# Kernel optimization log

Measured on AMD Instinct MI355X. Metric: run time of the kernel, lower is better.

Reference implementation:

```python
import jax
import jax.numpy as jnp
from jax import lax
import numpy as np

VOCAB = 50000
EMB = 32
HID = 32
LAYERS = 4
BATCH = 8192
SEQ = 111


def setup_inputs() -> dict:
    key = jax.random.key(0)
    ks = jax.random.split(key, 12)
    s = 0.1
    x = jax.random.randint(ks[0], (BATCH, SEQ), 0, VOCAB, dtype=jnp.int64 if jax.config.read('jax_enable_x64') else jnp.int32)
    emb = jax.random.normal(ks[1], (VOCAB, EMB), jnp.float32) * s
    # stacked per-layer LSTM weights; layer-0 input dim == EMB == HID so stacking is valid
    Wih = jax.random.normal(ks[2], (LAYERS, 4 * HID, EMB), jnp.float32) * s
    Whh = jax.random.normal(ks[3], (LAYERS, 4 * HID, HID), jnp.float32) * s
    bih = jax.random.normal(ks[4], (LAYERS, 4 * HID), jnp.float32) * s
    bhh = jax.random.normal(ks[5], (LAYERS, 4 * HID), jnp.float32) * s
    Wa = jax.random.normal(ks[6], (HID, 1), jnp.float32) * s
    ba = jax.random.normal(ks[7], (1,), jnp.float32) * s
    W1 = jax.random.normal(ks[8], (HID, 32), jnp.float32) * s
    b1 = jax.random.normal(ks[9], (32,), jnp.float32) * s
    W2 = jax.random.normal(ks[10], (32, 3), jnp.float32) * s
    b2 = jax.random.normal(ks[11], (3,), jnp.float32) * s
    return {"x": x, "emb": emb, "Wih": Wih, "Whh": Whh, "bih": bih, "bhh": bhh,
            "Wa": Wa, "ba": ba, "W1": W1, "b1": b1, "W2": W2, "b2": b2}


def _lstm_layer(x, Wih, Whh, bih, bhh):
    # x: [B, T, D] -> [B, T, H]; PyTorch gate order: i, f, g, o
    B = x.shape[0]
    H = Whh.shape[1]
    # precompute the input contribution for all timesteps (one big GEMM)
    xg = jnp.einsum('btd,gd->btg', x, Wih) + bih + bhh  # [B, T, 4H]

    def step(carry, xg_t):
        h, c = carry
        z = xg_t + h @ Whh.T  # [B, 4H]
        i, f, g, o = jnp.split(z, 4, axis=-1)
        c = jax.nn.sigmoid(f) * c + jax.nn.sigmoid(i) * jnp.tanh(g)
        h = jax.nn.sigmoid(o) * jnp.tanh(c)
        return (h, c), h

    init = (jnp.zeros((B, H), x.dtype), jnp.zeros((B, H), x.dtype))
    _, hs = lax.scan(step, init, jnp.swapaxes(xg, 0, 1))  # hs: [T, B, H]
    return jnp.swapaxes(hs, 0, 1)


def reference(x, emb, Wih, Whh, bih, bhh, Wa, ba, W1, b1, W2, b2):
    h = emb[x]  # [B, T, E]
    for l in range(Wih.shape[0]):  # fixed 4 layers
        h = _lstm_layer(h, Wih[l], Whh[l], bih[l], bhh[l])
    scores = h @ Wa + ba                       # [B, T, 1]
    attn = jax.nn.softmax(scores, axis=1)      # softmax over time
    context = jnp.sum(h * attn, axis=1)        # [B, H]
    hid = jnp.tanh(context @ W1 + b1)          # dropout is identity at eval
    return hid @ W2 + b2                       # [B, 3]
```

## Files before the change

kernel.cpp:

```cpp
#include <hip/hip_runtime.h>

#define TSEQ 111
#define L2E 1.44269504088896340736f
#define TWO_L2E 2.88539008177792680472f

using f32x4  = __attribute__((ext_vector_type(4))) float;
using f32x2  = __attribute__((ext_vector_type(2))) float;
using short8 = __attribute__((ext_vector_type(8))) short;

union FragU { unsigned u[4]; uint4 v; short8 s; };

__device__ __forceinline__ float fexp2(float x) { return __builtin_amdgcn_exp2f(x); }
__device__ __forceinline__ float frcp(float x)  { return __builtin_amdgcn_rcpf(x); }
__device__ __forceinline__ float tanh2(float zs) { return 1.f - 2.f * frcp(1.f + fexp2(zs + zs)); }
__device__ __forceinline__ f32x2 exp2v(f32x2 x) { f32x2 r; r[0] = fexp2(x[0]); r[1] = fexp2(x[1]); return r; }
__device__ __forceinline__ f32x2 rcpv(f32x2 x)  { f32x2 r; r[0] = frcp(x[0]); r[1] = frcp(x[1]); return r; }

__device__ __forceinline__ unsigned rnd_bf16(float w) {
  unsigned u = __float_as_uint(w);
  return (u + 0x7fffu + ((u >> 16) & 1u)) >> 16;
}
__device__ __forceinline__ unsigned cvtpk(float a, float b) {
  unsigned r;
  asm("v_cvt_pk_bf16_f32 %0, %1, %2" : "=v"(r) : "v"(a), "v"(b));
  return r;
}

__global__ __launch_bounds__(512, 4) void lstm_fused(
    const int* __restrict__ x, const float* __restrict__ emb,
    const float* __restrict__ Wih, const float* __restrict__ Whh,
    const float* __restrict__ bih, const float* __restrict__ bhh,
    const float* __restrict__ Wa, const float* __restrict__ W1,
    const float* __restrict__ b1, const float* __restrict__ W2,
    const float* __restrict__ b2, float* __restrict__ out)
{
  __shared__ __align__(16) unsigned short hb[2 * 4 * 512];

  const int tid  = threadIdx.x;
  const int wvu  = __builtin_amdgcn_readfirstlane(tid) >> 6;
  const int l    = wvu >> 1;
  const int hf   = wvu & 1;
  const int lane = tid & 63;
  const int c    = lane & 15;
  const int q    = lane >> 4;
  const int gcc  = (c & 3) ^ (c >> 2);
  const int rowbase = blockIdx.x * 16;
  const int xrow = (rowbase + c) * TSEQ;

  const int rdOff = c * 32 + ((q ^ gcc) << 3);
  const int wrOff = c * 32 + ((((2 * hf + (q >> 1)) ^ gcc) << 3) | ((q & 1) << 2));

  FragU wihf[4], whhf[4];
#pragma unroll
  for (int g = 0; g < 4; ++g) {
    const float sj = (g == 2) ? TWO_L2E : -L2E;
    const int wr = 32 * g + 16 * hf + c;
    const float* srcI = Wih + l * 4096 + wr * 32 + 8 * q;
    const float* srcH = Whh + l * 4096 + wr * 32 + 8 * q;
#pragma unroll
    for (int p = 0; p < 4; ++p) {
      wihf[g].u[p] = rnd_bf16(srcI[2 * p] * sj) | (rnd_bf16(srcI[2 * p + 1] * sj) << 16);
      whhf[g].u[p] = rnd_bf16(srcH[2 * p] * sj) | (rnd_bf16(srcH[2 * p + 1] * sj) << 16);
    }
  }
  f32x4 bvv[4];
#pragma unroll
  for (int g = 0; g < 4; ++g) {
    const float sj = (g == 2) ? TWO_L2E : -L2E;
    const int bi = l * 128 + 32 * g + 16 * hf + 4 * q;
#pragma unroll
    for (int e = 0; e < 4; ++e)
      bvv[g][e] = (bih[bi + e] + bhh[bi + e]) * sj;
  }

  FragU wahA, walA;
#pragma unroll
  for (int p = 0; p < 4; ++p) { wahA.u[p] = 0u; walA.u[p] = 0u; }
  if (l == 3) {
#pragma unroll
    for (int p = 0; p < 4; ++p) {
      const int k0 = 8 * q + 2 * p;
      float w0 = Wa[k0] * L2E, w1 = Wa[k0 + 1] * L2E;
      unsigned h0 = rnd_bf16(w0), h1b = rnd_bf16(w1);
      wahA.u[p] = h0 | (h1b << 16);
      float l0v = w0 - __uint_as_float(h0 << 16);
      float l1v = w1 - __uint_as_float(h1b << 16);
      walA.u[p] = rnd_bf16(l0v) | (rnd_bf16(l1v) << 16);
    }
  }

  f32x2 cs2[2];
  cs2[0] = (f32x2){0.f, 0.f}; cs2[1] = (f32x2){0.f, 0.f};
  float mr = -1e30f, sr = 0.f, cx[4];
#pragma unroll
  for (int e = 0; e < 4; ++e) cx[e] = 0.f;

  for (int i = tid; i < 2 * 4 * 512 / 2; i += 512) ((unsigned*)hb)[i] = 0u;

  float4 emA = make_float4(0.f, 0.f, 0.f, 0.f), emB = emA;
  int idxn = 0;
  if (l == 0) {
    int i0 = x[xrow];
    emA = *(const float4*)(emb + i0 * 32 + 8 * q);
    emB = *(const float4*)(emb + i0 * 32 + 8 * q + 4);
    idxn = x[xrow + 1];
  }
  __syncthreads();

  if (blockIdx.x & 1) {
    __builtin_amdgcn_s_sleep(15);
    __builtin_amdgcn_s_sleep(15);
  }

#pragma unroll 2
  for (int s = 0; s < TSEQ + 4; ++s) {
    const int t = s - l;
    const bool active = ((unsigned)t < (unsigned)TSEQ);
    const int rp = (s + 1) & 1;
    const int wp = s & 1;
    const bool doAtt = (l == 3) && (s >= 4);

    FragU fi, fh;
    __builtin_amdgcn_s_setprio(1);
    if (active) {
      if (l == 0) {
        fi.u[0] = cvtpk(emA.x, emA.y); fi.u[1] = cvtpk(emA.z, emA.w);
        fi.u[2] = cvtpk(emB.x, emB.y); fi.u[3] = cvtpk(emB.z, emB.w);
        if (t + 1 < TSEQ) {
          emA = *(const float4*)(emb + idxn * 32 + 8 * q);
          emB = *(const float4*)(emb + idxn * 32 + 8 * q + 4);
        }
        if (t + 2 < TSEQ) idxn = x[xrow + t + 2];
      } else {
        fi.v = *(const uint4*)(hb + (rp * 4 + (l - 1)) * 512 + rdOff);
      }
    }
    if (active || doAtt)
      fh.v = *(const uint4*)(hb + (rp * 4 + l) * 512 + rdOff);

    f32x4 acc[4];
    if (active) {
#pragma unroll
      for (int g = 0; g < 4; ++g) {
        acc[g] = __builtin_amdgcn_mfma_f32_16x16x32_bf16(wihf[g].s, fi.s, bvv[g], 0, 0, 0);
        acc[g] = __builtin_amdgcn_mfma_f32_16x16x32_bf16(whhf[g].s, fh.s, acc[g], 0, 0, 0);
      }
    }
    f32x4 sacc;
    if (doAtt) {
      f32x4 z = {0.f, 0.f, 0.f, 0.f};
      sacc = __builtin_amdgcn_mfma_f32_16x16x32_bf16(wahA.s, fh.s, z, 0, 0, 0);
      sacc = __builtin_amdgcn_mfma_f32_16x16x32_bf16(walA.s, fh.s, sacc, 0, 0, 0);
    }
    __builtin_amdgcn_s_setprio(0);

    if (active) {
      float hv[4];
      const f32x2 one = {1.f, 1.f};
      const f32x2 tl2 = {TWO_L2E, TWO_L2E};
#pragma unroll
      for (int pr2 = 0; pr2 < 2; ++pr2) {
        const int e0 = 2 * pr2;
        f32x2 va; va[0] = acc[0][e0]; va[1] = acc[0][e0 + 1];
        f32x2 vm; vm[0] = acc[1][e0]; vm[1] = acc[1][e0 + 1];
        f32x2 vb; vb[0] = acc[2][e0]; vb[1] = acc[2][e0 + 1];
        f32x2 vp; vp[0] = acc[3][e0]; vp[1] = acc[3][e0 + 1];
        f32x2 ea = exp2v(va), em_ = exp2v(vm), eb = exp2v(vb), ep = exp2v(vp);
        f32x2 P  = (one + ea) * (one + eb);
        f32x2 M1 = one + em_;
        f32x2 num = cs2[pr2] * P + (eb - one) * M1;
        f32x2 cn = num * rcpv(M1 * P);
        cs2[pr2] = cn;
        f32x2 qa = cn * tl2;
        qa[0] = fminf(qa[0], 80.f); qa[1] = fminf(qa[1], 80.f);
        f32x2 qv = exp2v(qa);
        f32x2 hvv = (qv - one) * rcpv((one + ep) * (one + qv));
        hv[e0] = hvv[0]; hv[e0 + 1] = hvv[1];
      }

      *(uint2*)(hb + (wp * 4 + l) * 512 + wrOff) =
          make_uint2(cvtpk(hv[0], hv[1]), cvtpk(hv[2], hv[3]));
    }

    if (doAtt) {
      float pf = sacc[0];
      float mn = fmaxf(mr, pf);
      float sc = fexp2(mr - mn);
      float pr = fexp2(pf - mn);
      sr = sr * sc + pr;
#pragma unroll
      for (int p = 0; p < 2; ++p) {
        unsigned w = fh.u[2 * hf + p];
        cx[2 * p]     = cx[2 * p]     * sc + pr * __uint_as_float(w << 16);
        cx[2 * p + 1] = cx[2 * p + 1] * sc + pr * __uint_as_float(w & 0xffff0000u);
      }
      mr = mn;
    }

    asm volatile("s_waitcnt lgkmcnt(0)\n\ts_barrier" ::: "memory");
  }

  __syncthreads();

  float* cb = (float*)hb;
  if (l == 3) {
    float inv = frcp(sr);
#pragma unroll
    for (int e = 0; e < 4; ++e)
      cb[c * 33 + 8 * q + 4 * hf + e] = cx[e] * inv;
  }
  __syncthreads();
  if (wvu != 6) return;

  float a0[4], a1[4];
  {
    float bb0 = b1[c], bb1 = b1[c + 16];
#pragma unroll
    for (int e = 0; e < 4; ++e) { a0[e] = bb0; a1[e] = bb1; }
    for (int j = 0; j < 32; ++j) {
      float w0 = W1[j * 32 + c];
      float w1 = W1[j * 32 + c + 16];
#pragma unroll
      for (int e = 0; e < 4; ++e) {
        float cr = cb[(4 * q + e) * 33 + j];
        a0[e] = fmaf(cr, w0, a0[e]);
        a1[e] = fmaf(cr, w1, a1[e]);
      }
    }
  }
  float o0[4], o1[4], o2[4];
  {
    float w20 = W2[c * 3 + 0], w21 = W2[c * 3 + 1], w22 = W2[c * 3 + 2];
    float w30 = W2[(c + 16) * 3 + 0], w31 = W2[(c + 16) * 3 + 1], w32 = W2[(c + 16) * 3 + 2];
#pragma unroll
    for (int e = 0; e < 4; ++e) {
      float h0 = tanh2(a0[e] * L2E);
      float hB = tanh2(a1[e] * L2E);
      o0[e] = h0 * w20 + hB * w30;
      o1[e] = h0 * w21 + hB * w31;
      o2[e] = h0 * w22 + hB * w32;
    }
  }
#pragma unroll
  for (int mk = 1; mk <= 8; mk <<= 1) {
#pragma unroll
    for (int e = 0; e < 4; ++e) {
      o0[e] += __shfl_xor(o0[e], mk, 64);
      o1[e] += __shfl_xor(o1[e], mk, 64);
      o2[e] += __shfl_xor(o2[e], mk, 64);
    }
  }
  if (c < 3) {
    float bb = b2[c];
#pragma unroll
    for (int e = 0; e < 4; ++e) {
      float v = (c == 0) ? o0[e] : ((c == 1) ? o1[e] : o2[e]);
      out[(rowbase + 4 * q + e) * 3 + c] = v + bb;
    }
  }
}

extern "C" void kernel_launch(void* const* d_in, const int* in_sizes, int n_in,
                              void* d_out, int out_size, void* d_ws, size_t ws_size,
                              hipStream_t stream) {
  const int*   x   = (const int*)d_in[0];
  const float* emb = (const float*)d_in[1];
  const float* Wih = (const float*)d_in[2];
  const float* Whh = (const float*)d_in[3];
  const float* bih = (const float*)d_in[4];
  const float* bhh = (const float*)d_in[5];
  const float* Wa  = (const float*)d_in[6];
  const float* W1  = (const float*)d_in[8];
  const float* b1  = (const float*)d_in[9];
  const float* W2  = (const float*)d_in[10];
  const float* b2  = (const float*)d_in[11];
  float* out = (float*)d_out;

  lstm_fused<<<512, 512, 0, stream>>>(x, emb, Wih, Whh, bih, bhh, Wa, W1, b1, W2, b2, out);
}
```

Before: 164.5 us.

## Process LSTM layers in 8-timestep chunks with one wave per layer

Each layer is now handled by a single wave that keeps the recurrent state in registers. Hidden states pass between layers through shared memory in chunks of 8 timesteps, so the block barriers drop from one per timestep to one per chunk. The block shrinks from 512 to 256 threads, and the per-layer wave pair and swizzled LDS layout go away, along with the s_sleep staggering and setprio. In exchange each wave does twice the MFMA and transcendental work per step, serially, with higher register pressure. The skew between layers is now a whole chunk, and the last chunk is padded.

```diff
diff --git a/kernel.cpp b/kernel.cpp
--- a/kernel.cpp
+++ b/kernel.cpp
@@ -1,6 +1,9 @@
 #include <hip/hip_runtime.h>
 
 #define TSEQ 111
+#define CT 8
+#define NCH 14
+#define NSS (NCH + 3)
 #define L2E 1.44269504088896340736f
 #define TWO_L2E 2.88539008177792680472f
 
@@ -20,13 +23,16 @@
   unsigned u = __float_as_uint(w);
   return (u + 0x7fffu + ((u >> 16) & 1u)) >> 16;
 }
+__device__ __forceinline__ unsigned pk2(float a, float b) {
+  return rnd_bf16(a) | (rnd_bf16(b) << 16);
+}
 __device__ __forceinline__ unsigned cvtpk(float a, float b) {
   unsigned r;
   asm("v_cvt_pk_bf16_f32 %0, %1, %2" : "=v"(r) : "v"(a), "v"(b));
   return r;
 }
 
-__global__ __launch_bounds__(512, 4) void lstm_fused(
+__global__ __launch_bounds__(256, 2) void lstm_fused(
     const int* __restrict__ x, const float* __restrict__ emb,
     const float* __restrict__ Wih, const float* __restrict__ Whh,
     const float* __restrict__ bih, const float* __restrict__ bhh,
@@ -34,40 +40,33 @@
     const float* __restrict__ b1, const float* __restrict__ W2,
     const float* __restrict__ b2, float* __restrict__ out)
 {
-  __shared__ __align__(16) unsigned short hb[2 * 4 * 512];
+  __shared__ __align__(16) unsigned short buf[2 * 3 * CT * 512];
 
   const int tid  = threadIdx.x;
-  const int wvu  = __builtin_amdgcn_readfirstlane(tid) >> 6;
-  const int l    = wvu >> 1;
-  const int hf   = wvu & 1;
+  const int l    = __builtin_amdgcn_readfirstlane(tid) >> 6;
   const int lane = tid & 63;
   const int c    = lane & 15;
   const int q    = lane >> 4;
-  const int gcc  = (c & 3) ^ (c >> 2);
   const int rowbase = blockIdx.x * 16;
   const int xrow = (rowbase + c) * TSEQ;
 
-  const int rdOff = c * 32 + ((q ^ gcc) << 3);
-  const int wrOff = c * 32 + ((((2 * hf + (q >> 1)) ^ gcc) << 3) | ((q & 1) << 2));
-
-  FragU wihf[4], whhf[4];
-#pragma unroll
-  for (int g = 0; g < 4; ++g) {
-    const float sj = (g == 2) ? TWO_L2E : -L2E;
-    const int wr = 32 * g + 16 * hf + c;
-    const float* srcI = Wih + l * 4096 + wr * 32 + 8 * q;
-    const float* srcH = Whh + l * 4096 + wr * 32 + 8 * q;
-#pragma unroll
-    for (int p = 0; p < 4; ++p) {
-      wihf[g].u[p] = rnd_bf16(srcI[2 * p] * sj) | (rnd_bf16(srcI[2 * p + 1] * sj) << 16);
-      whhf[g].u[p] = rnd_bf16(srcH[2 * p] * sj) | (rnd_bf16(srcH[2 * p + 1] * sj) << 16);
-    }
-  }
-  f32x4 bvv[4];
-#pragma unroll
-  for (int g = 0; g < 4; ++g) {
-    const float sj = (g == 2) ? TWO_L2E : -L2E;
-    const int bi = l * 128 + 32 * g + 16 * hf + 4 * q;
+  FragU wih[8], whh[8];
+  f32x4 bvv[8];
+#pragma unroll
+  for (int g = 0; g < 8; ++g) {
+    const float sj = ((g >> 1) == 2) ? TWO_L2E : -L2E;
+    const int wr = 16 * g + c;
+    const float* WI = Wih + l * 4096 + wr * 32;
+    const float* WH = Whh + l * 4096 + wr * 32;
+    float4 ia = *(const float4*)(WI + 4 * q);
+    float4 ib = *(const float4*)(WI + 16 + 4 * q);
+    float4 ha = *(const float4*)(WH + 4 * q);
+    float4 hb = *(const float4*)(WH + 16 + 4 * q);
+    wih[g].u[0] = pk2(ia.x * sj, ia.y * sj); wih[g].u[1] = pk2(ia.z * sj, ia.w * sj);
+    wih[g].u[2] = pk2(ib.x * sj, ib.y * sj); wih[g].u[3] = pk2(ib.z * sj, ib.w * sj);
+    whh[g].u[0] = pk2(ha.x * sj, ha.y * sj); whh[g].u[1] = pk2(ha.z * sj, ha.w * sj);
+    whh[g].u[2] = pk2(hb.x * sj, hb.y * sj); whh[g].u[3] = pk2(hb.z * sj, hb.w * sj);
+    const int bi = l * 128 + 16 * g + 4 * q;
 #pragma unroll
     for (int e = 0; e < 4; ++e)
       bvv[g][e] = (bih[bi + e] + bhh[bi + e]) * sj;
@@ -77,140 +76,178 @@
 #pragma unroll
   for (int p = 0; p < 4; ++p) { wahA.u[p] = 0u; walA.u[p] = 0u; }
   if (l == 3) {
+    float wv[8];
+    float4 wa0 = *(const float4*)(Wa + 4 * q);
+    float4 wa1 = *(const float4*)(Wa + 16 + 4 * q);
+    wv[0] = wa0.x; wv[1] = wa0.y; wv[2] = wa0.z; wv[3] = wa0.w;
+    wv[4] = wa1.x; wv[5] = wa1.y; wv[6] = wa1.z; wv[7] = wa1.w;
 #pragma unroll
     for (int p = 0; p < 4; ++p) {
-      const int k0 = 8 * q + 2 * p;
-      float w0 = Wa[k0] * L2E, w1 = Wa[k0 + 1] * L2E;
-      unsigned h0 = rnd_bf16(w0), h1b = rnd_bf16(w1);
-      wahA.u[p] = h0 | (h1b << 16);
+      float w0 = wv[2 * p] * L2E, w1 = wv[2 * p + 1] * L2E;
+      unsigned h0 = rnd_bf16(w0), h1 = rnd_bf16(w1);
+      wahA.u[p] = h0 | (h1 << 16);
       float l0v = w0 - __uint_as_float(h0 << 16);
-      float l1v = w1 - __uint_as_float(h1b << 16);
+      float l1v = w1 - __uint_as_float(h1 << 16);
       walA.u[p] = rnd_bf16(l0v) | (rnd_bf16(l1v) << 16);
     }
   }
 
-  f32x2 cs2[2];
-  cs2[0] = (f32x2){0.f, 0.f}; cs2[1] = (f32x2){0.f, 0.f};
-  float mr = -1e30f, sr = 0.f, cx[4];
-#pragma unroll
-  for (int e = 0; e < 4; ++e) cx[e] = 0.f;
-
-  for (int i = tid; i < 2 * 4 * 512 / 2; i += 512) ((unsigned*)hb)[i] = 0u;
-
-  float4 emA = make_float4(0.f, 0.f, 0.f, 0.f), emB = emA;
-  int idxn = 0;
+  f32x2 csE[2], csO[2];
+  csE[0] = (f32x2){0.f, 0.f}; csE[1] = (f32x2){0.f, 0.f};
+  csO[0] = (f32x2){0.f, 0.f}; csO[1] = (f32x2){0.f, 0.f};
+  FragU fh;
+  fh.u[0] = 0u; fh.u[1] = 0u; fh.u[2] = 0u; fh.u[3] = 0u;
+  float mr = -1e30f, sr = 0.f;
+  float cxE[4], cxO[4];
+#pragma unroll
+  for (int e = 0; e < 4; ++e) { cxE[e] = 0.f; cxO[e] = 0.f; }
+
+  int idxc[CT];
   if (l == 0) {
-    int i0 = x[xrow];
-    emA = *(const float4*)(emb + i0 * 32 + 8 * q);
-    emB = *(const float4*)(emb + i0 * 32 + 8 * q + 4);
-    idxn = x[xrow + 1];
+#pragma unroll
+    for (int j = 0; j < CT; ++j) idxc[j] = x[xrow + j];
   }
   __syncthreads();
 
-  if (blockIdx.x & 1) {
-    __builtin_amdgcn_s_sleep(15);
-    __builtin_amdgcn_s_sleep(15);
-  }
-
-#pragma unroll 2
-  for (int s = 0; s < TSEQ + 4; ++s) {
-    const int t = s - l;
-    const bool active = ((unsigned)t < (unsigned)TSEQ);
+  for (int s = 0; s < NSS; ++s) {
+    const int ch = s - l;
+    const bool active = ((unsigned)ch < (unsigned)NCH);
     const int rp = (s + 1) & 1;
     const int wp = s & 1;
-    const bool doAtt = (l == 3) && (s >= 4);
-
-    FragU fi, fh;
-    __builtin_amdgcn_s_setprio(1);
+
+    FragU fiU[CT];
+    float4 emE[4], emO[4];
+    int idxn[CT];
+
+    if (l == 0) {
+      if (active) {
+#pragma unroll
+        for (int j = 0; j < 4; ++j) {
+          emE[j] = *(const float4*)(emb + idxc[j] * 32 + 4 * q);
+          emO[j] = *(const float4*)(emb + idxc[j] * 32 + 16 + 4 * q);
+        }
+#pragma unroll
+        for (int j = 0; j < CT; ++j) {
+          int tt = (ch + 1) * CT + j;
+          tt = tt > TSEQ - 1 ? TSEQ - 1 : tt;
+          idxn[j] = x[xrow + tt];
+        }
+      }
+    } else if (active) {
+      const unsigned short* bp =
+          buf + ((rp * 3 + (l - 1)) * CT) * 512 + c * 32 + q * 8;
+#pragma unroll
+      for (int j = 0; j < CT; ++j)
+        fiU[j].v = *(const uint4*)(bp + j * 512);
+    }
+
     if (active) {
+#pragma unroll
+      for (int tau = 0; tau < CT; ++tau) {
+        FragU fi;
+        if (l == 0) {
+          float4 eE = emE[tau & 3], eO = emO[tau & 3];
+          fi.u[0] = cvtpk(eE.x, eE.y); fi.u[1] = cvtpk(eE.z, eE.w);
+          fi.u[2] = cvtpk(eO.x, eO.y); fi.u[3] = cvtpk(eO.z, eO.w);
+          if (tau + 4 < CT) {
+            emE[tau & 3] = *(const float4*)(emb + idxc[tau + 4] * 32 + 4 * q);
+            emO[tau & 3] = *(const float4*)(emb + idxc[tau + 4] * 32 + 16 + 4 * q);
+          }
+        } else {
+          fi = fiU[tau];
+        }
+
+        f32x4 acc[8];
+#pragma unroll
+        for (int g = 0; g < 8; ++g)
+          acc[g] = __builtin_amdgcn_mfma_f32_16x16x32_bf16(wih[g].s, fi.s, bvv[g], 0, 0, 0);
+#pragma unroll
+        for (int g = 0; g < 8; ++g)
+          acc[g] = __builtin_amdgcn_mfma_f32_16x16x32_bf16(whh[g].s, fh.s, acc[g], 0, 0, 0);
+
+        float hvE[4], hvO[4];
+        const f32x2 one = {1.f, 1.f};
+        const f32x2 tl2 = {TWO_L2E, TWO_L2E};
+#pragma unroll
+        for (int p2 = 0; p2 < 2; ++p2) {
+          const int e0 = 2 * p2;
+          {
+            f32x2 vi; vi[0] = acc[0][e0]; vi[1] = acc[0][e0 + 1];
+            f32x2 vf; vf[0] = acc[2][e0]; vf[1] = acc[2][e0 + 1];
+            f32x2 vg; vg[0] = acc[4][e0]; vg[1] = acc[4][e0 + 1];
+            f32x2 vo; vo[0] = acc[6][e0]; vo[1] = acc[6][e0 + 1];
+            f32x2 ea = exp2v(vi), em_ = exp2v(vf), eb = exp2v(vg), ep = exp2v(vo);
+            f32x2 P  = (one + ea) * (one + eb);
+            f32x2 M1 = one + em_;
+            f32x2 cn = (csE[p2] * P + (eb - one) * M1) * rcpv(M1 * P);
+            csE[p2] = cn;
+            f32x2 qa = cn * tl2;
+            qa[0] = fminf(qa[0], 80.f); qa[1] = fminf(qa[1], 80.f);
+            f32x2 qv = exp2v(qa);
+            f32x2 hvv = (qv - one) * rcpv((one + ep) * (one + qv));
+            hvE[e0] = hvv[0]; hvE[e0 + 1] = hvv[1];
+          }
+          {
+            f32x2 vi; vi[0] = acc[1][e0]; vi[1] = acc[1][e0 + 1];
+            f32x2 vf; vf[0] = acc[3][e0]; vf[1] = acc[3][e0 + 1];
+            f32x2 vg; vg[0] = acc[5][e0]; vg[1] = acc[5][e0 + 1];
+            f32x2 vo; vo[0] = acc[7][e0]; vo[1] = acc[7][e0 + 1];
+            f32x2 ea = exp2v(vi), em_ = exp2v(vf), eb = exp2v(vg), ep = exp2v(vo);
+            f32x2 P  = (one + ea) * (one + eb);
+            f32x2 M1 = one + em_;
+            f32x2 cn = (csO[p2] * P + (eb - one) * M1) * rcpv(M1 * P);
+            csO[p2] = cn;
+            f32x2 qa = cn * tl2;
+            qa[0] = fminf(qa[0], 80.f); qa[1] = fminf(qa[1], 80.f);
+            f32x2 qv = exp2v(qa);
+            f32x2 hvv = (qv - one) * rcpv((one + ep) * (one + qv));
+            hvO[e0] = hvv[0]; hvO[e0 + 1] = hvv[1];
+          }
+        }
+
+        fh.u[0] = cvtpk(hvE[0], hvE[1]); fh.u[1] = cvtpk(hvE[2], hvE[3]);
+        fh.u[2] = cvtpk(hvO[0], hvO[1]); fh.u[3] = cvtpk(hvO[2], hvO[3]);
+
+        if (l < 3)
+          *(uint4*)(buf + ((wp * 3 + l) * CT + tau) * 512 + c * 32 + q * 8) = fh.v;
+
+        if (l == 3 && ch * CT + tau < TSEQ) {
+          f32x4 z = {0.f, 0.f, 0.f, 0.f};
+          f32x4 sacc = __builtin_amdgcn_mfma_f32_16x16x32_bf16(wahA.s, fh.s, z, 0, 0, 0);
+          sacc = __builtin_amdgcn_mfma_f32_16x16x32_bf16(walA.s, fh.s, sacc, 0, 0, 0);
+          float pf = sacc[0];
+          float mn = fmaxf(mr, pf);
+          float scl = fexp2(mr - mn);
+          float pr = fexp2(pf - mn);
+          sr = sr * scl + pr;
+#pragma unroll
+          for (int e = 0; e < 4; ++e) {
+            cxE[e] = cxE[e] * scl + pr * hvE[e];
+            cxO[e] = cxO[e] * scl + pr * hvO[e];
+          }
+          mr = mn;
+        }
+      }
       if (l == 0) {
-        fi.u[0] = cvtpk(emA.x, emA.y); fi.u[1] = cvtpk(emA.z, emA.w);
-        fi.u[2] = cvtpk(emB.x, emB.y); fi.u[3] = cvtpk(emB.z, emB.w);
-        if (t + 1 < TSEQ) {
-          emA = *(const float4*)(emb + idxn * 32 + 8 * q);
-          emB = *(const float4*)(emb + idxn * 32 + 8 * q + 4);
-        }
-        if (t + 2 < TSEQ) idxn = x[xrow + t + 2];
-      } else {
-        fi.v = *(const uint4*)(hb + (rp * 4 + (l - 1)) * 512 + rdOff);
+#pragma unroll
+        for (int j = 0; j < CT; ++j) idxc[j] = idxn[j];
       }
     }
-    if (active || doAtt)
-      fh.v = *(const uint4*)(hb + (rp * 4 + l) * 512 + rdOff);
-
-    f32x4 acc[4];
-    if (active) {
-#pragma unroll
-      for (int g = 0; g < 4; ++g) {
-        acc[g] = __builtin_amdgcn_mfma_f32_16x16x32_bf16(wihf[g].s, fi.s, bvv[g], 0, 0, 0);
-        acc[g] = __builtin_amdgcn_mfma_f32_16x16x32_bf16(whhf[g].s, fh.s, acc[g], 0, 0, 0);
-      }
-    }
-    f32x4 sacc;
-    if (doAtt) {
-      f32x4 z = {0.f, 0.f, 0.f, 0.f};
-      sacc = __builtin_amdgcn_mfma_f32_16x16x32_bf16(wahA.s, fh.s, z, 0, 0, 0);
-      sacc = __builtin_amdgcn_mfma_f32_16x16x32_bf16(walA.s, fh.s, sacc, 0, 0, 0);
-    }
-    __builtin_amdgcn_s_setprio(0);
-
-    if (active) {
-      float hv[4];
-      const f32x2 one = {1.f, 1.f};
-      const f32x2 tl2 = {TWO_L2E, TWO_L2E};
-#pragma unroll
-      for (int pr2 = 0; pr2 < 2; ++pr2) {
-        const int e0 = 2 * pr2;
-        f32x2 va; va[0] = acc[0][e0]; va[1] = acc[0][e0 + 1];
-        f32x2 vm; vm[0] = acc[1][e0]; vm[1] = acc[1][e0 + 1];
-        f32x2 vb; vb[0] = acc[2][e0]; vb[1] = acc[2][e0 + 1];
-        f32x2 vp; vp[0] = acc[3][e0]; vp[1] = acc[3][e0 + 1];
-        f32x2 ea = exp2v(va), em_ = exp2v(vm), eb = exp2v(vb), ep = exp2v(vp);
-        f32x2 P  = (one + ea) * (one + eb);
-        f32x2 M1 = one + em_;
-        f32x2 num = cs2[pr2] * P + (eb - one) * M1;
-        f32x2 cn = num * rcpv(M1 * P);
-        cs2[pr2] = cn;
-        f32x2 qa = cn * tl2;
-        qa[0] = fminf(qa[0], 80.f); qa[1] = fminf(qa[1], 80.f);
-        f32x2 qv = exp2v(qa);
-        f32x2 hvv = (qv - one) * rcpv((one + ep) * (one + qv));
-        hv[e0] = hvv[0]; hv[e0 + 1] = hvv[1];
-      }
-
-      *(uint2*)(hb + (wp * 4 + l) * 512 + wrOff) =
-          make_uint2(cvtpk(hv[0], hv[1]), cvtpk(hv[2], hv[3]));
-    }
-
-    if (doAtt) {
-      float pf = sacc[0];
-      float mn = fmaxf(mr, pf);
-      float sc = fexp2(mr - mn);
-      float pr = fexp2(pf - mn);
-      sr = sr * sc + pr;
-#pragma unroll
-      for (int p = 0; p < 2; ++p) {
-        unsigned w = fh.u[2 * hf + p];
-        cx[2 * p]     = cx[2 * p]     * sc + pr * __uint_as_float(w << 16);
-        cx[2 * p + 1] = cx[2 * p + 1] * sc + pr * __uint_as_float(w & 0xffff0000u);
-      }
-      mr = mn;
-    }
 
     asm volatile("s_waitcnt lgkmcnt(0)\n\ts_barrier" ::: "memory");
   }
 
-  __syncthreads();
-
-  float* cb = (float*)hb;
+  float* cb = (float*)buf;
   if (l == 3) {
     float inv = frcp(sr);
 #pragma unroll
-    for (int e = 0; e < 4; ++e)
-      cb[c * 33 + 8 * q + 4 * hf + e] = cx[e] * inv;
+    for (int e = 0; e < 4; ++e) {
+      cb[c * 33 + 4 * q + e]      = cxE[e] * inv;
+      cb[c * 33 + 16 + 4 * q + e] = cxO[e] * inv;
+    }
   }
   __syncthreads();
-  if (wvu != 6) return;
+  if (l != 1) return;
 
   float a0[4], a1[4];
   {
@@ -276,5 +313,5 @@
   const float* b2  = (const float*)d_in[11];
   float* out = (float*)d_out;
 
-  lstm_fused<<<512, 512, 0, stream>>>(x, emb, Wih, Whh, bih, bhh, Wa, W1, b1, W2, b2, out);
-}
+  lstm_fused<<<512, 256, 0, stream>>>(x, emb, Wih, Whh, bih, bhh, Wa, W1, b1, W2, b2, out);
+}
```

New measurement: 180.6 us. 1.1x slower.
